# Kernel tuning notes

Measured on AMD Instinct MI355X. Metric: run time of the kernel, lower is better.

Reference implementation:

```python
import jax, jax.numpy as jnp
import numpy as np

DIMS = (128, 128, 128)
KERNEL_SIZE = 3
EPS = 1e-6


def setup_inputs() -> dict:
    key = jax.random.key(0)
    k1, _ = jax.random.split(key)
    bs, n = 16, 100000
    # raw voxel-space coordinates in [0, dims) as expected by norm_grid_space
    point_cloud = jax.random.uniform(k1, (bs, n, 3), dtype=jnp.float32) * jnp.asarray(DIMS, jnp.float32)
    sigma = jnp.asarray(0.5, jnp.float32)  # learnable smoothing width
    return {"point_cloud": point_cloud, "sigma": sigma}


def _pc_voxels(points, dims):
    # points are normalized to (-0.5, 0.5); trilinear splat into [bs, X, Y, Z]
    bs, n, _ = points.shape
    X, Y, Z = dims
    vox = jnp.asarray(dims, points.dtype)
    valid = jnp.all((points < 0.5 - EPS) & (points > -0.5 + EPS), axis=-1)  # [bs, n]
    grid = (points + 0.5) * (vox - 1.0)                                   # [bs, n, 3]
    gf = jnp.floor(grid)
    gi = gf.astype(jnp.int32)
    r = grid - gf                                                          # frac part
    # 8 trilinear corners, offsets in {0,1}^3
    corners = jnp.asarray([[k, j, i] for k in (0, 1) for j in (0, 1) for i in (0, 1)], jnp.int32)  # [8,3]
    # weight per corner = prod_axis (r if offset==1 else 1-r)
    w = jnp.prod(jnp.where(corners[None, None].astype(bool), r[:, :, None, :], 1.0 - r[:, :, None, :]), axis=-1)  # [bs,n,8]
    w = w * valid[:, :, None].astype(points.dtype)
    idx = gi[:, :, None, :] + corners[None, None]                          # [bs,n,8,3]
    idx = jnp.where(valid[:, :, None, None], idx, 0)                      # safe index for masked pts
    b = jnp.arange(bs, dtype=jnp.int32)[:, None, None]
    flat = ((b * X + idx[..., 0]) * Y + idx[..., 1]) * Z + idx[..., 2]     # [bs,n,8]
    vox_flat = jnp.zeros(bs * X * Y * Z, points.dtype).at[flat.reshape(-1)].add(w.reshape(-1))
    return jnp.clip(vox_flat.reshape(bs, X, Y, Z), 0.0, 1.0)


def _smooth(voxels, sigma):
    # separable 1D Gaussian conv along z, y, x (same order as the torch code)
    K = KERNEL_SIZE
    x = jnp.arange((-K) // 2 + 1.0, K // 2 + 1.0, dtype=voxels.dtype)  # e.g. [-1,0,1]
    kern = jnp.exp(-x ** 2 / (2.0 * sigma ** 2))
    kern = kern / kern.sum()
    pad = K // 2
    v = voxels
    for axis in (3, 2, 1):  # z, y, x
        pads = [(pad, pad) if a == axis else (0, 0) for a in range(4)]
        vp = jnp.pad(v, pads)
        L = v.shape[axis]
        v = sum(kern[t] * jax.lax.slice_in_dim(vp, t, t + L, axis=axis) for t in range(K))
    return jnp.clip(v, 0.0, 1.0)


def reference(point_cloud, sigma):
    vox = jnp.asarray(DIMS, point_cloud.dtype)
    pcn = point_cloud / vox - 0.5  # norm_grid_space: (p - d/2)/d
    voxels = _pc_voxels(pcn, DIMS)
    smoothed = _smooth(voxels, sigma)
    return smoothed[:, None]  # [bs, 1, X, Y, Z]
```

## Files before the change

kernel.cpp:

```cpp
#include <hip/hip_runtime.h>

#define GD 128
#define PLANE (GD * GD)
#define EPSF 1e-6f

#define BSX 8
#define BSY 32
#define BSZ 32
#define NBX 16
#define NBY 4
#define NBZ 4
#define BINS_PER_BATCH (NBX * NBY * NBZ)
#define N_BINS_TOTAL (16 * BINS_PER_BATCH)
#define CAP 768
#define CNT_STRIDE 16

#define TY 16
#define XC 16

__device__ __forceinline__ float clamp01(float v) {
    return fminf(fmaxf(v, 0.0f), 1.0f);
}

__global__ __launch_bounds__(256) void bin_kernel(
    const float* __restrict__ pc, int n_per_b, int total,
    unsigned* __restrict__ counts, unsigned* __restrict__ entries) {
    int i = blockIdx.x * blockDim.x + threadIdx.x;
    if (i >= total) return;

    float px = pc[3 * i + 0];
    float py = pc[3 * i + 1];
    float pz = pc[3 * i + 2];

    const float inv = 1.0f / 128.0f;
    float nx = px * inv - 0.5f;
    float ny = py * inv - 0.5f;
    float nz = pz * inv - 0.5f;

    const float hi = 0.5f - EPSF;
    const float lo = -0.5f + EPSF;
    bool valid = (nx < hi) && (nx > lo) &&
                 (ny < hi) && (ny > lo) &&
                 (nz < hi) && (nz > lo);
    if (!valid) return;

    float gx = (nx + 0.5f) * 127.0f;
    float gy = (ny + 0.5f) * 127.0f;
    float gz = (nz + 0.5f) * 127.0f;
    int ix = (int)floorf(gx);
    int iy = (int)floorf(gy);
    int iz = (int)floorf(gz);

    int b = i / n_per_b;
    int bx0 = ix >> 3, bx1 = (ix + 1) >> 3;
    int by0 = iy >> 5, by1 = (iy + 1) >> 5;
    int bz0 = iz >> 5, bz1 = (iz + 1) >> 5;

    for (int bx = bx0; bx <= bx1; ++bx)
        for (int by = by0; by <= by1; ++by)
            for (int bz = bz0; bz <= bz1; ++bz) {
                int bin = ((b * NBX + bx) * NBY + by) * NBZ + bz;
                unsigned slot = atomicAdd(&counts[bin * CNT_STRIDE], 1u);
                if (slot < CAP)
                    entries[(size_t)bin * CAP + slot] = (unsigned)i;
            }
}

__global__ __launch_bounds__(256) void splat_bin_kernel(
    const unsigned* __restrict__ counts, const unsigned* __restrict__ entries,
    const float* __restrict__ pc, float* __restrict__ out) {
    __shared__ float sub[BSX * BSY * BSZ];
    int bin = blockIdx.x;
    int tid = threadIdx.x;

    float4* s4 = (float4*)sub;
    #pragma unroll
    for (int t = tid; t < (BSX * BSY * BSZ) / 4; t += 256)
        s4[t] = make_float4(0.0f, 0.0f, 0.0f, 0.0f);
    __syncthreads();

    int batch = bin >> 8;
    int bx = (bin >> 4) & (NBX - 1);
    int by = (bin >> 2) & (NBY - 1);
    int bz = bin & (NBZ - 1);
    int x0 = bx * BSX, y0 = by * BSY, z0 = bz * BSZ;

    unsigned cnt = counts[bin * CNT_STRIDE];
    if (cnt > CAP) cnt = CAP;
    const unsigned* ep = entries + (size_t)bin * CAP;

    const float inv = 1.0f / 128.0f;
    for (unsigned e = tid; e < cnt; e += 256) {
        unsigned pi = ep[e];
        float px = pc[3 * pi + 0];
        float py = pc[3 * pi + 1];
        float pz = pc[3 * pi + 2];
        float gx = (px * inv - 0.5f + 0.5f) * 127.0f;
        float gy = (py * inv - 0.5f + 0.5f) * 127.0f;
        float gz = (pz * inv - 0.5f + 0.5f) * 127.0f;
        float fx = floorf(gx), fy = floorf(gy), fz = floorf(gz);
        int ix = (int)fx, iy = (int)fy, iz = (int)fz;
        float rx = gx - fx, ry = gy - fy, rz = gz - fz;
        int lx0 = ix - x0, ly0 = iy - y0, lz0 = iz - z0;
        float wx[2] = {1.0f - rx, rx};
        float wy[2] = {1.0f - ry, ry};
        float wz[2] = {1.0f - rz, rz};
        #pragma unroll
        for (int dx = 0; dx < 2; ++dx) {
            int lx = lx0 + dx;
            if ((unsigned)lx >= BSX) continue;
            #pragma unroll
            for (int dy = 0; dy < 2; ++dy) {
                int ly = ly0 + dy;
                if ((unsigned)ly >= BSY) continue;
                #pragma unroll
                for (int dz = 0; dz < 2; ++dz) {
                    int lz = lz0 + dz;
                    if ((unsigned)lz >= BSZ) continue;
                    atomicAdd(&sub[(lx * BSY + ly) * BSZ + lz],
                              wx[dx] * wy[dy] * wz[dz]);
                }
            }
        }
    }
    __syncthreads();

    #pragma unroll
    for (int t = tid; t < (BSX * BSY * BSZ) / 4; t += 256) {
        float4 v = s4[t];
        v.x = clamp01(v.x); v.y = clamp01(v.y);
        v.z = clamp01(v.z); v.w = clamp01(v.w);
        int l = t * 4;
        int lx = l >> 10;
        int r  = l & 1023;
        int ly = r >> 5;
        int lz = r & 31;
        size_t o = (((size_t)(batch * GD + x0 + lx)) * GD + (y0 + ly)) * GD
                   + (z0 + lz);
        *(float4*)&out[o] = v;
    }
}

__global__ __launch_bounds__(256) void smooth_fused_kernel(
    const float* __restrict__ src, float* __restrict__ dst,
    const float* __restrict__ sigma_p) {
    __shared__ float p[(TY + 2) * GD];

    float s = sigma_p[0];
    float e = expf(-1.0f / (2.0f * s * s));
    float norm = 1.0f / (1.0f + 2.0f * e);
    float a = e * norm;
    float c = norm;

    int bid = blockIdx.x;
    int b  = bid >> 6;
    int yt = (bid >> 3) & 7;
    int xc = bid & 7;
    int y0 = yt * TY;
    int x0 = xc * XC;

    int tid = threadIdx.x;
    int z   = tid & 127;
    int yh  = tid >> 7;
    int yb  = yh * 8;

    const float* srcb = src + ((size_t)b << 21);
    float* dstb       = dst + ((size_t)b << 21);

    float prev[8], cur[8], nxt[8];
    #pragma unroll
    for (int k = 0; k < 8; ++k) { prev[k] = 0.f; cur[k] = 0.f; nxt[k] = 0.f; }

    for (int xs = x0 - 1; xs <= x0 + XC; ++xs) {
        #pragma unroll
        for (int k = 0; k < 8; ++k) { prev[k] = cur[k]; cur[k] = nxt[k]; }

        if (xs >= 0 && xs < GD) {
            const float4* sl4 = (const float4*)(srcb + ((size_t)xs << 14));
            for (int t4 = tid; t4 < (TY + 2) * GD / 4; t4 += 256) {
                int yy = y0 - 1 + (t4 >> 5);
                float4 v = make_float4(0.f, 0.f, 0.f, 0.f);
                if ((unsigned)yy < (unsigned)GD) v = sl4[(yy << 5) | (t4 & 31)];
                ((float4*)p)[t4] = v;
            }
            __syncthreads();

            float sreg[10];
            #pragma unroll
            for (int j = 0; j < 10; ++j) {
                const float* row = &p[(yb + j) << 7];
                float l = (z > 0)      ? row[z - 1] : 0.0f;
                float m = row[z];
                float r = (z < GD - 1) ? row[z + 1] : 0.0f;
                sreg[j] = a * (l + r) + c * m;
            }
            #pragma unroll
            for (int k = 0; k < 8; ++k)
                nxt[k] = a * (sreg[k] + sreg[k + 2]) + c * sreg[k + 1];
            __syncthreads();
        } else {
            #pragma unroll
            for (int k = 0; k < 8; ++k) nxt[k] = 0.0f;
        }

        int xo = xs - 1;
        if (xo >= x0 && xo < x0 + XC) {
            float* dsl = dstb + ((size_t)xo << 14);
            #pragma unroll
            for (int k = 0; k < 8; ++k) {
                float r = a * (prev[k] + nxt[k]) + c * cur[k];
                dsl[((y0 + yb + k) << 7) | z] = clamp01(r);
            }
        }
    }
}

__global__ __launch_bounds__(256) void splat_kernel(
    const float* __restrict__ pc, int n_per_b, int total,
    float* __restrict__ vox) {
    int i = blockIdx.x * blockDim.x + threadIdx.x;
    if (i >= total) return;

    float px = pc[3 * i + 0];
    float py = pc[3 * i + 1];
    float pz = pc[3 * i + 2];

    const float inv = 1.0f / 128.0f;
    float nx = px * inv - 0.5f;
    float ny = py * inv - 0.5f;
    float nz = pz * inv - 0.5f;

    const float hi = 0.5f - EPSF;
    const float lo = -0.5f + EPSF;
    bool valid = (nx < hi) && (nx > lo) &&
                 (ny < hi) && (ny > lo) &&
                 (nz < hi) && (nz > lo);
    if (!valid) return;

    float gx = (nx + 0.5f) * 127.0f;
    float gy = (ny + 0.5f) * 127.0f;
    float gz = (nz + 0.5f) * 127.0f;
    float fx = floorf(gx), fy = floorf(gy), fz = floorf(gz);
    int ix = (int)fx, iy = (int)fy, iz = (int)fz;
    float rx = gx - fx, ry = gy - fy, rz = gz - fz;

    int b = i / n_per_b;
    size_t base = ((size_t)((b * GD + ix) * GD + iy)) * GD + iz;

    float wx0 = 1.0f - rx, wx1 = rx;
    float wy0 = 1.0f - ry, wy1 = ry;
    float wz0 = 1.0f - rz, wz1 = rz;

    atomicAdd(&vox[base],                  wx0 * wy0 * wz0);
    atomicAdd(&vox[base + 1],              wx0 * wy0 * wz1);
    atomicAdd(&vox[base + GD],             wx0 * wy1 * wz0);
    atomicAdd(&vox[base + GD + 1],         wx0 * wy1 * wz1);
    atomicAdd(&vox[base + PLANE],          wx1 * wy0 * wz0);
    atomicAdd(&vox[base + PLANE + 1],      wx1 * wy0 * wz1);
    atomicAdd(&vox[base + PLANE + GD],     wx1 * wy1 * wz0);
    atomicAdd(&vox[base + PLANE + GD + 1], wx1 * wy1 * wz1);
}

__global__ __launch_bounds__(256) void smooth_zy_kernel(
    float* __restrict__ vox, const float* __restrict__ sigma_p, int clamp_in) {
    __shared__ float p[GD][GD];
    __shared__ float q[GD][GD];

    float s = sigma_p[0];
    float e = expf(-1.0f / (2.0f * s * s));
    float norm = 1.0f / (1.0f + 2.0f * e);
    float a = e * norm;
    float c = norm;

    float* plane = vox + (size_t)blockIdx.x * PLANE;

    for (int t = threadIdx.x; t < PLANE / 4; t += 256) {
        float4 v = ((const float4*)plane)[t];
        if (clamp_in) {
            v.x = clamp01(v.x); v.y = clamp01(v.y);
            v.z = clamp01(v.z); v.w = clamp01(v.w);
        }
        ((float4*)p)[t] = v;
    }
    __syncthreads();

    for (int t = threadIdx.x; t < PLANE; t += 256) {
        int y = t >> 7, z = t & 127;
        float l = (z > 0)   ? p[y][z - 1] : 0.0f;
        float r = (z < 127) ? p[y][z + 1] : 0.0f;
        q[y][z] = a * (l + r) + c * p[y][z];
    }
    __syncthreads();

    for (int t = threadIdx.x; t < PLANE; t += 256) {
        int y = t >> 7, z = t & 127;
        float u = (y > 0)   ? q[y - 1][z] : 0.0f;
        float d = (y < 127) ? q[y + 1][z] : 0.0f;
        plane[t] = a * (u + d) + c * q[y][z];
    }
}

__global__ __launch_bounds__(256) void smooth_x_kernel(
    float* __restrict__ vox, const float* __restrict__ sigma_p, int n_cols) {
    int idx = blockIdx.x * blockDim.x + threadIdx.x;
    if (idx >= n_cols) return;

    float s = sigma_p[0];
    float e = expf(-1.0f / (2.0f * s * s));
    float norm = 1.0f / (1.0f + 2.0f * e);
    float a = e * norm;
    float c = norm;

    int b  = idx >> 14;
    int yz = idx & (PLANE - 1);
    float* col = vox + ((size_t)b << 21) + yz;

    float prev = 0.0f;
    float cur  = col[0];
    #pragma unroll 4
    for (int x = 0; x < GD; ++x) {
        float nxt = (x < GD - 1) ? col[(size_t)(x + 1) << 14] : 0.0f;
        float r = a * (prev + nxt) + c * cur;
        col[(size_t)x << 14] = clamp01(r);
        prev = cur;
        cur  = nxt;
    }
}

extern "C" void kernel_launch(void* const* d_in, const int* in_sizes, int n_in,
                              void* d_out, int out_size, void* d_ws, size_t ws_size,
                              hipStream_t stream) {
    const float* pc    = (const float*)d_in[0];
    const float* sigma = (const float*)d_in[1];
    float* out = (float*)d_out;

    int total   = in_sizes[0] / 3;
    int bs      = out_size / (GD * GD * GD);
    int n_per_b = total / bs;
    int n_cols  = bs * PLANE;

    size_t counts_bytes  = (size_t)N_BINS_TOTAL * CNT_STRIDE * sizeof(unsigned);
    size_t entries_bytes = (size_t)N_BINS_TOTAL * CAP * sizeof(unsigned);
    size_t grid_bytes    = (size_t)16 * GD * GD * GD * sizeof(float);
    size_t need_small = counts_bytes + entries_bytes;
    size_t need_full  = need_small + grid_bytes;

    if (bs == 16 && ws_size >= need_full) {
        unsigned* counts  = (unsigned*)d_ws;
        unsigned* entries = (unsigned*)((char*)d_ws + counts_bytes);
        float* gridws     = (float*)((char*)d_ws + need_small);
        hipMemsetAsync(counts, 0, counts_bytes, stream);
        bin_kernel<<<(total + 255) / 256, 256, 0, stream>>>(
            pc, n_per_b, total, counts, entries);
        splat_bin_kernel<<<N_BINS_TOTAL, 256, 0, stream>>>(
            counts, entries, pc, gridws);
        smooth_fused_kernel<<<bs * 8 * 8, 256, 0, stream>>>(gridws, out, sigma);
    } else if (bs == 16 && ws_size >= need_small) {
        unsigned* counts  = (unsigned*)d_ws;
        unsigned* entries = (unsigned*)((char*)d_ws + counts_bytes);
        hipMemsetAsync(counts, 0, counts_bytes, stream);
        bin_kernel<<<(total + 255) / 256, 256, 0, stream>>>(
            pc, n_per_b, total, counts, entries);
        splat_bin_kernel<<<N_BINS_TOTAL, 256, 0, stream>>>(
            counts, entries, pc, out);
        smooth_zy_kernel<<<bs * GD, 256, 0, stream>>>(out, sigma, 0);
        smooth_x_kernel<<<(n_cols + 255) / 256, 256, 0, stream>>>(out, sigma, n_cols);
    } else {
        hipMemsetAsync(out, 0, (size_t)out_size * sizeof(float), stream);
        splat_kernel<<<(total + 255) / 256, 256, 0, stream>>>(
            pc, n_per_b, total, out);
        smooth_zy_kernel<<<bs * GD, 256, 0, stream>>>(out, sigma, 1);
        smooth_x_kernel<<<(n_cols + 255) / 256, 256, 0, stream>>>(out, sigma, n_cols);
    }
}
```

Baseline: 349.2 us.

## Aggregate bin counts in shared memory and halve smoothing x-chunk

```diff
diff --git a/kernel.cpp b/kernel.cpp
--- a/kernel.cpp
+++ b/kernel.cpp
@@ -16,54 +16,87 @@
 #define CNT_STRIDE 16
 
 #define TY 16
-#define XC 16
+#define XC 8
 
 __device__ __forceinline__ float clamp01(float v) {
     return fminf(fmaxf(v, 0.0f), 1.0f);
 }
 
-__global__ __launch_bounds__(256) void bin_kernel(
-    const float* __restrict__ pc, int n_per_b, int total,
+__global__ __launch_bounds__(1024) void bin_kernel(
+    const float* __restrict__ pc, int n_per_b,
     unsigned* __restrict__ counts, unsigned* __restrict__ entries) {
-    int i = blockIdx.x * blockDim.x + threadIdx.x;
-    if (i >= total) return;
-
-    float px = pc[3 * i + 0];
-    float py = pc[3 * i + 1];
-    float pz = pc[3 * i + 2];
-
-    const float inv = 1.0f / 128.0f;
-    float nx = px * inv - 0.5f;
-    float ny = py * inv - 0.5f;
-    float nz = pz * inv - 0.5f;
-
-    const float hi = 0.5f - EPSF;
-    const float lo = -0.5f + EPSF;
-    bool valid = (nx < hi) && (nx > lo) &&
-                 (ny < hi) && (ny > lo) &&
-                 (nz < hi) && (nz > lo);
-    if (!valid) return;
-
-    float gx = (nx + 0.5f) * 127.0f;
-    float gy = (ny + 0.5f) * 127.0f;
-    float gz = (nz + 0.5f) * 127.0f;
-    int ix = (int)floorf(gx);
-    int iy = (int)floorf(gy);
-    int iz = (int)floorf(gz);
-
-    int b = i / n_per_b;
+    __shared__ unsigned lcnt[BINS_PER_BATCH];
+    __shared__ unsigned lbase[BINS_PER_BATCH];
+
+    int tid = threadIdx.x;
+    int b   = blockIdx.y;
+    int p   = blockIdx.x * 1024 + tid;
+
+    if (tid < BINS_PER_BATCH) lcnt[tid] = 0;
+    __syncthreads();
+
+    bool valid = false;
+    int ix = 0, iy = 0, iz = 0;
+    int i = b * n_per_b + p;
+    if (p < n_per_b) {
+        float px = pc[3 * i + 0];
+        float py = pc[3 * i + 1];
+        float pz = pc[3 * i + 2];
+
+        const float inv = 1.0f / 128.0f;
+        float nx = px * inv - 0.5f;
+        float ny = py * inv - 0.5f;
+        float nz = pz * inv - 0.5f;
+
+        const float hi = 0.5f - EPSF;
+        const float lo = -0.5f + EPSF;
+        valid = (nx < hi) && (nx > lo) &&
+                (ny < hi) && (ny > lo) &&
+                (nz < hi) && (nz > lo);
+        if (valid) {
+            float gx = (nx + 0.5f) * 127.0f;
+            float gy = (ny + 0.5f) * 127.0f;
+            float gz = (nz + 0.5f) * 127.0f;
+            ix = (int)floorf(gx);
+            iy = (int)floorf(gy);
+            iz = (int)floorf(gz);
+        }
+    }
+
     int bx0 = ix >> 3, bx1 = (ix + 1) >> 3;
     int by0 = iy >> 5, by1 = (iy + 1) >> 5;
     int bz0 = iz >> 5, bz1 = (iz + 1) >> 5;
 
-    for (int bx = bx0; bx <= bx1; ++bx)
-        for (int by = by0; by <= by1; ++by)
-            for (int bz = bz0; bz <= bz1; ++bz) {
-                int bin = ((b * NBX + bx) * NBY + by) * NBZ + bz;
-                unsigned slot = atomicAdd(&counts[bin * CNT_STRIDE], 1u);
-                if (slot < CAP)
-                    entries[(size_t)bin * CAP + slot] = (unsigned)i;
-            }
+    if (valid) {
+        for (int bx = bx0; bx <= bx1; ++bx)
+            for (int by = by0; by <= by1; ++by)
+                for (int bz = bz0; bz <= bz1; ++bz)
+                    atomicAdd(&lcnt[(bx * NBY + by) * NBZ + bz], 1u);
+    }
+    __syncthreads();
+
+    if (tid < BINS_PER_BATCH) {
+        unsigned n = lcnt[tid];
+        unsigned base = 0;
+        if (n)
+            base = atomicAdd(&counts[(b * BINS_PER_BATCH + tid) * CNT_STRIDE], n);
+        lbase[tid] = base;
+        lcnt[tid] = 0;
+    }
+    __syncthreads();
+
+    if (valid) {
+        for (int bx = bx0; bx <= bx1; ++bx)
+            for (int by = by0; by <= by1; ++by)
+                for (int bz = bz0; bz <= bz1; ++bz) {
+                    int lb = (bx * NBY + by) * NBZ + bz;
+                    unsigned slot = atomicAdd(&lcnt[lb], 1u);
+                    unsigned idx = lbase[lb] + slot;
+                    if (idx < CAP)
+                        entries[(size_t)(b * BINS_PER_BATCH + lb) * CAP + idx]
+                            = (unsigned)i;
+                }
+    }
 }
 
 __global__ __launch_bounds__(256) void splat_bin_kernel(
@@ -153,9 +186,9 @@
     float c = norm;
 
     int bid = blockIdx.x;
-    int b  = bid >> 6;
-    int yt = (bid >> 3) & 7;
-    int xc = bid & 7;
+    int b  = bid >> 7;
+    int yt = (bid >> 4) & 7;
+    int xc = bid & 15;
     int y0 = yt * TY;
     int x0 = xc * XC;
 
@@ -345,22 +378,22 @@
     size_t need_small = counts_bytes + entries_bytes;
     size_t need_full  = need_small + grid_bytes;
 
+    dim3 bin_grid((n_per_b + 1023) / 1024, bs);
+
     if (bs == 16 && ws_size >= need_full) {
         unsigned* counts  = (unsigned*)d_ws;
         unsigned* entries = (unsigned*)((char*)d_ws + counts_bytes);
         float* gridws     = (float*)((char*)d_ws + need_small);
         hipMemsetAsync(counts, 0, counts_bytes, stream);
-        bin_kernel<<<(total + 255) / 256, 256, 0, stream>>>(
-            pc, n_per_b, total, counts, entries);
+        bin_kernel<<<bin_grid, 1024, 0, stream>>>(pc, n_per_b, counts, entries);
         splat_bin_kernel<<<N_BINS_TOTAL, 256, 0, stream>>>(
             counts, entries, pc, gridws);
-        smooth_fused_kernel<<<bs * 8 * 8, 256, 0, stream>>>(gridws, out, sigma);
+        smooth_fused_kernel<<<bs * 8 * 16, 256, 0, stream>>>(gridws, out, sigma);
     } else if (bs == 16 && ws_size >= need_small) {
         unsigned* counts  = (unsigned*)d_ws;
         unsigned* entries = (unsigned*)((char*)d_ws + counts_bytes);
         hipMemsetAsync(counts, 0, counts_bytes, stream);
-        bin_kernel<<<(total + 255) / 256, 256, 0, stream>>>(
-            pc, n_per_b, total, counts, entries);
+        bin_kernel<<<bin_grid, 1024, 0, stream>>>(pc, n_per_b, counts, entries);
         splat_bin_kernel<<<N_BINS_TOTAL, 256, 0, stream>>>(
             counts, entries, pc, out);
         smooth_zy_kernel<<<bs * GD, 256, 0, stream>>>(out, sigma, 0);
```

Measured after the change: 290.6 us. 1.2x faster.
